# Optimization experiments

Hardware: AMD Instinct MI355X
Metric: run time of the kernel (lower is better)

Reference implementation:

```python
import jax, jax.numpy as jnp
import numpy as np

N_EMBD, D_INNER, DT_RANK, D_CONV, D_STATE, SEQ_LEN = 2048, 4096, 128, 4, 16, 2048


def setup_inputs() -> dict:
    key = jax.random.key(0)
    ks = jax.random.split(key, 8)
    sc = lambda fan_in: 1.0 / np.sqrt(fan_in)
    x = jax.random.normal(ks[0], (SEQ_LEN, N_EMBD), dtype=jnp.float32)
    in_proj_w = jax.random.normal(ks[1], (2 * D_INNER, N_EMBD), jnp.float32) * sc(N_EMBD)
    in_proj_b = jnp.zeros((2 * D_INNER,), jnp.float32)
    conv_w = jax.random.normal(ks[2], (D_INNER, 1, D_CONV), jnp.float32) * sc(D_CONV)
    conv_b = jnp.zeros((D_INNER,), jnp.float32)
    ssm_in_w = jax.random.normal(ks[3], (DT_RANK + 2 * D_STATE, D_INNER), jnp.float32) * sc(D_INNER)
    delta_w = jax.random.normal(ks[4], (D_INNER, DT_RANK), jnp.float32) * sc(DT_RANK)
    # A_log init exactly as module: repeat(arange(1,d_state+1), d_inner).reshape(d_inner,d_state)
    A_log = jnp.log(jnp.repeat(jnp.arange(1, D_STATE + 1), D_INNER).reshape(D_INNER, D_STATE).astype(jnp.float32))
    D = jnp.ones((D_INNER,), jnp.float32)
    out_w = jax.random.normal(ks[5], (N_EMBD, D_INNER), jnp.float32) * sc(D_INNER)
    out_b = jnp.zeros((N_EMBD,), jnp.float32)
    return {"x": x, "in_proj_w": in_proj_w, "in_proj_b": in_proj_b, "conv_w": conv_w,
            "conv_b": conv_b, "ssm_in_w": ssm_in_w, "delta_w": delta_w, "A_log": A_log,
            "D": D, "out_w": out_w, "out_b": out_b}


def selective_scan(u, delta, A, B, C, D):
    # u, delta: (L, di); A: (di, ds); B, C: (L, ds); D: (di,)
    dA = jnp.exp(delta[:, :, None] * A[None, :, :])                # (L, di, ds)
    dBu = delta[:, :, None] * B[:, None, :] * u[:, :, None]        # (L, di, ds)

    def step(h, inp):
        dA_t, dBu_t, C_t = inp
        h = dA_t * h + dBu_t                                       # (di, ds)
        y = jnp.einsum('ds,s->d', h, C_t)
        return h, y

    h0 = jnp.zeros((u.shape[1], A.shape[1]), u.dtype)
    _, ys = jax.lax.scan(step, h0, (dA, dBu, C))
    return ys + u * D                                              # (L, di)


def mamba_block(x, in_proj_w, in_proj_b, conv_w, conv_b, ssm_in_w, delta_w, A_log, D, out_w, out_b):
    L = x.shape[0]
    xr = x @ in_proj_w.T + in_proj_b                               # (L, 2*di)
    xi, res = jnp.split(xr, 2, axis=-1)
    # depthwise causal conv1d: left-pad d_conv-1 (== first L outputs of symmetric pad)
    xc = jax.lax.conv_general_dilated(
        xi.T[None],                                                # (1, di, L)
        conv_w,                                                    # (di, 1, k)
        window_strides=(1,), padding=[(D_CONV - 1, 0)],
        feature_group_count=D_INNER)[0] + conv_b[:, None]
    xc = jax.nn.silu(xc.T)                                         # (L, di)
    # SSM
    A = -jnp.exp(A_log)
    dbc = xc @ ssm_in_w.T                                          # (L, dt_rank + 2*ds)
    delta, B, C = jnp.split(dbc, [DT_RANK, DT_RANK + D_STATE], axis=-1)
    delta = jax.nn.softplus(delta @ delta_w.T)                     # (L, di)
    y = selective_scan(xc, delta, A, B, C, D)
    y = y * jax.nn.silu(res)
    return y @ out_w.T + out_b                                     # (L, n_embd)


def reference(x, in_proj_w, in_proj_b, conv_w, conv_b, ssm_in_w, delta_w, A_log, D, out_w, out_b):
    return mamba_block(x, in_proj_w, in_proj_b, conv_w, conv_b, ssm_in_w, delta_w, A_log, D, out_w, out_b)
```

## Files before the change

### kernel.cpp

```cpp
#include <hip/hip_runtime.h>
#include <cstdint>
#include <cstddef>


typedef __bf16 bf16x8 __attribute__((ext_vector_type(8)));
typedef float f32x4 __attribute__((ext_vector_type(4)));

#define GLDS16(g, l)                                        \
  __builtin_amdgcn_global_load_lds(                         \
      (__attribute__((address_space(1))) void*)(g),         \
      (__attribute__((address_space(3))) void*)(l), 16, 0, 0)

#define FENCE() asm volatile("" ::: "memory")
#define BARRIER()                      \
  do {                                 \
    FENCE();                           \
    __builtin_amdgcn_s_barrier();      \
    FENCE();                           \
  } while (0)

static __device__ __forceinline__ unsigned short f2b(float f) {
  unsigned int x = __builtin_bit_cast(unsigned int, f);
  x += 0x7fffu + ((x >> 16) & 1u);
  return (unsigned short)(x >> 16);
}

static __device__ __forceinline__ float b2f(unsigned short u) {
  return __builtin_bit_cast(float, (unsigned int)u << 16);
}

static __device__ __forceinline__ float sigmoidf_fast(float x) {
  return 1.0f / (1.0f + __expf(-x));
}

struct CastArgs {
  const float* src[5];
  unsigned short* dst[5];
  int n4[5];
};

__global__ __launch_bounds__(256) void cast_multi(CastArgs a) {
  const int stride = gridDim.x * 256;
  const int t = blockIdx.x * 256 + threadIdx.x;
#pragma unroll
  for (int k = 0; k < 5; ++k) {
    const float4* src = reinterpret_cast<const float4*>(a.src[k]);
    ushort4* dst = reinterpret_cast<ushort4*>(a.dst[k]);
    const int n4 = a.n4[k];
    for (int i = t; i < n4; i += stride) {
      float4 v = src[i];
      ushort4 o;
      o.x = f2b(v.x); o.y = f2b(v.y); o.z = f2b(v.z); o.w = f2b(v.w);
      dst[i] = o;
    }
  }
}

template <int MODE>
__global__ __launch_bounds__(512) void gemm256_bt(
    const unsigned short* __restrict__ A, const unsigned short* __restrict__ B,
    float* __restrict__ Cp, unsigned short* __restrict__ xib,
    unsigned short* __restrict__ rsb, const float* __restrict__ bias,
    int M, int N, int K, int Kslice) {
  __shared__ __align__(16) unsigned short lds[65536];
  const int tid = threadIdx.x;
  const int l = tid & 63;
  const int w = tid >> 6;
  const int wr = w >> 2;
  const int wc = w & 3;

  const int nwg = gridDim.x * gridDim.y;
  const int q = nwg >> 3;
  int flat = blockIdx.x + gridDim.x * blockIdx.y;
  flat = (flat & 7) * q + (flat >> 3);
  const int bx = flat % gridDim.x;
  const int by = flat / gridDim.x;

  const long brow = (long)bx * 256;
  const long bcol = (long)by * 256;
  const int ks = blockIdx.z;
  const int NT = Kslice >> 6;

  f32x4 acc[8][4] = {};

  const unsigned short* Ab = A + (size_t)brow * K + (size_t)ks * Kslice;
  const unsigned short* Bb = B + (size_t)bcol * K + (size_t)ks * Kslice;
  size_t soff[4];
  int doff[4];
#pragma unroll
  for (int i = 0; i < 4; ++i) {
    int idx = i * 512 + tid;
    int r = idx >> 3, s = idx & 7;
    soff[i] = (size_t)r * K + (size_t)((s ^ (r & 7)) << 3);
    doff[i] = idx * 8;
  }

  auto stage = [&](int kt, int buf) {
    const int k0 = kt << 6;
#pragma unroll
    for (int i = 0; i < 4; ++i)
      GLDS16(Ab + soff[i] + k0, &lds[buf * 32768 + doff[i]]);
#pragma unroll
    for (int i = 0; i < 4; ++i)
      GLDS16(Bb + soff[i] + k0, &lds[buf * 32768 + 16384 + doff[i]]);
  };

  const int hi = l >> 4, lo7 = l & 7;
  const int sw0 = ((0 + hi) ^ lo7) << 3;
  const int sw1 = ((4 + hi) ^ lo7) << 3;
  const int rowA = wr * 128 + (l & 15);
  const int colB = wc * 64 + (l & 15);

  stage(0, 0);
  stage(1, 1);

  int buf = 0;
  for (int kt = 0; kt < NT; ++kt) {
    const bool last = (kt == NT - 1);
    if (last) {
      asm volatile("s_waitcnt vmcnt(0)" ::: "memory");
    } else {
      asm volatile("s_waitcnt vmcnt(8)" ::: "memory");
    }
    BARRIER();
    const int bb = buf * 32768;
    bf16x8 a0[8], b0[4];
#pragma unroll
    for (int m = 0; m < 8; ++m)
      a0[m] = *reinterpret_cast<const bf16x8*>(&lds[bb + (rowA + m * 16) * 64 + sw0]);
#pragma unroll
    for (int n = 0; n < 4; ++n)
      b0[n] = *reinterpret_cast<const bf16x8*>(&lds[bb + 16384 + (colB + n * 16) * 64 + sw0]);
    __builtin_amdgcn_s_setprio(1);
#pragma unroll
    for (int m = 0; m < 8; ++m)
#pragma unroll
      for (int n = 0; n < 4; ++n)
        acc[m][n] = __builtin_amdgcn_mfma_f32_16x16x32_bf16(a0[m], b0[n], acc[m][n], 0, 0, 0);
    __builtin_amdgcn_s_setprio(0);
    bf16x8 a1[8], b1[4];
#pragma unroll
    for (int m = 0; m < 8; ++m)
      a1[m] = *reinterpret_cast<const bf16x8*>(&lds[bb + (rowA + m * 16) * 64 + sw1]);
#pragma unroll
    for (int n = 0; n < 4; ++n)
      b1[n] = *reinterpret_cast<const bf16x8*>(&lds[bb + 16384 + (colB + n * 16) * 64 + sw1]);
    asm volatile("s_waitcnt lgkmcnt(0)" ::: "memory");
    __builtin_amdgcn_sched_barrier(0);
    BARRIER();
    if (kt + 2 < NT) stage(kt + 2, buf);
    __builtin_amdgcn_s_setprio(1);
#pragma unroll
    for (int m = 0; m < 8; ++m)
#pragma unroll
      for (int n = 0; n < 4; ++n)
        acc[m][n] = __builtin_amdgcn_mfma_f32_16x16x32_bf16(a1[m], b1[n], acc[m][n], 0, 0, 0);
    __builtin_amdgcn_s_setprio(0);
    buf ^= 1;
  }

  const long r0 = brow + wr * 128 + (l >> 4) * 4;
  const long c0 = bcol + wc * 64 + (l & 15);
  if (MODE == 1) {
    float* Cb = Cp + (size_t)ks * M * N;
#pragma unroll
    for (int m = 0; m < 8; ++m)
#pragma unroll
      for (int n = 0; n < 4; ++n) {
        long col = c0 + n * 16;
#pragma unroll
        for (int r = 0; r < 4; ++r)
          Cb[(r0 + m * 16 + r) * (long)N + col] = acc[m][n][r];
      }
  } else {
#pragma unroll
    for (int m = 0; m < 8; ++m)
#pragma unroll
      for (int n = 0; n < 4; ++n) {
        long col = c0 + n * 16;
        float bv = bias[col];
        const bool isres = col >= 4096;
        long cc = isres ? col - 4096 : col;
#pragma unroll
        for (int r = 0; r < 4; ++r) {
          float v = acc[m][n][r] + bv;
          if (isres) {
            float s = v * sigmoidf_fast(v);
            rsb[(r0 + m * 16 + r) * 4096 + cc] = f2b(s);
          } else {
            xib[(r0 + m * 16 + r) * 4096 + cc] = f2b(v);
          }
        }
      }
  }
}

__global__ __launch_bounds__(256) void reduce4_bias(
    const float* __restrict__ part, const float* __restrict__ bias,
    float* __restrict__ out, int n4) {
  int stride = gridDim.x * 256;
  for (int f = blockIdx.x * 256 + threadIdx.x; f < n4; f += stride) {
    float4 s0 = reinterpret_cast<const float4*>(part)[f];
    float4 s1 = reinterpret_cast<const float4*>(part + 4194304ull)[f];
    float4 s2 = reinterpret_cast<const float4*>(part + 8388608ull)[f];
    float4 s3 = reinterpret_cast<const float4*>(part + 12582912ull)[f];
    float4 bv = reinterpret_cast<const float4*>(bias)[f & 511];
    float4 o;
    o.x = s0.x + s1.x + s2.x + s3.x + bv.x;
    o.y = s0.y + s1.y + s2.y + s3.y + bv.y;
    o.z = s0.z + s1.z + s2.z + s3.z + bv.z;
    o.w = s0.w + s1.w + s2.w + s3.w + bv.w;
    reinterpret_cast<float4*>(out)[f] = o;
  }
}

__global__ __launch_bounds__(256) void gemm_bt_sp(
    const unsigned short* __restrict__ A, const unsigned short* __restrict__ B,
    float* __restrict__ C, int M, int N, int K) {
  __shared__ __align__(16) unsigned short lA[128 * 32];
  __shared__ __align__(16) unsigned short lB[128 * 32];
  const int tid = threadIdx.x;
  const int l = tid & 63;
  const int w = tid >> 6;
  const int wr = w >> 1, wc = w & 1;
  const long brow = (long)blockIdx.x * 128;
  const long bcol = (long)blockIdx.y * 128;

  f32x4 acc[4][4] = {};

  const int srow = tid >> 2;
  const int scol = (tid & 3) * 8;

  const unsigned short* Ab = A + (size_t)brow * K;
  const unsigned short* Bb = B + (size_t)bcol * K;

  for (int k0 = 0; k0 < K; k0 += 32) {
#pragma unroll
    for (int j = 0; j < 2; ++j) {
      GLDS16(Ab + (size_t)(j * 64 + srow) * K + k0 + scol, &lA[j * 2048 + tid * 8]);
      GLDS16(Bb + (size_t)(j * 64 + srow) * K + k0 + scol, &lB[j * 2048 + tid * 8]);
    }
    __syncthreads();
    bf16x8 af[4], bfr[4];
#pragma unroll
    for (int mt = 0; mt < 4; ++mt)
      af[mt] = *reinterpret_cast<const bf16x8*>(
          &lA[(wr * 64 + mt * 16 + (l & 15)) * 32 + (l >> 4) * 8]);
#pragma unroll
    for (int nt = 0; nt < 4; ++nt)
      bfr[nt] = *reinterpret_cast<const bf16x8*>(
          &lB[(wc * 64 + nt * 16 + (l & 15)) * 32 + (l >> 4) * 8]);
#pragma unroll
    for (int mt = 0; mt < 4; ++mt)
#pragma unroll
      for (int nt = 0; nt < 4; ++nt)
        acc[mt][nt] = __builtin_amdgcn_mfma_f32_16x16x32_bf16(
            af[mt], bfr[nt], acc[mt][nt], 0, 0, 0);
    __syncthreads();
  }

  const long r0 = brow + wr * 64 + ((l >> 4) * 4);
  const long c0 = bcol + wc * 64 + (l & 15);
#pragma unroll
  for (int mt = 0; mt < 4; ++mt) {
#pragma unroll
    for (int nt = 0; nt < 4; ++nt) {
      long col = c0 + nt * 16;
#pragma unroll
      for (int r = 0; r < 4; ++r) {
        long row = r0 + mt * 16 + r;
        float v = acc[mt][nt][r];
        v = (v > 20.0f) ? v : log1pf(__expf(v));
        C[row * (long)N + col] = v;
      }
    }
  }
}

__global__ __launch_bounds__(256) void conv_silu_k(
    const unsigned short* __restrict__ xib, const float* __restrict__ cw,
    const float* __restrict__ cb, unsigned short* __restrict__ xcb) {
  const int d = blockIdx.x * 256 + threadIdx.x;
  const int t0 = blockIdx.y * 128;
  const float4 wv = *reinterpret_cast<const float4*>(cw + (size_t)d * 4);
  const float bv = cb[d];
  float xm3 = (t0 >= 3) ? b2f(xib[(size_t)(t0 - 3) * 4096 + d]) : 0.0f;
  float xm2 = (t0 >= 2) ? b2f(xib[(size_t)(t0 - 2) * 4096 + d]) : 0.0f;
  float xm1 = (t0 >= 1) ? b2f(xib[(size_t)(t0 - 1) * 4096 + d]) : 0.0f;
  for (int tt = 0; tt < 128; ++tt) {
    const size_t t = (size_t)t0 + tt;
    float xt = b2f(xib[t * 4096 + d]);
    float a = bv + wv.x * xm3 + wv.y * xm2 + wv.z * xm1 + wv.w * xt;
    float s = a * sigmoidf_fast(a);
    xcb[t * 4096 + d] = f2b(s);
    xm3 = xm2; xm2 = xm1; xm1 = xt;
  }
}

__global__ __launch_bounds__(256) void gemm_dbc(
    const unsigned short* __restrict__ A, const unsigned short* __restrict__ B,
    float* __restrict__ part) {
  __shared__ __align__(16) unsigned short lA[64 * 32];
  __shared__ __align__(16) unsigned short lB[160 * 32];
  const int tid = threadIdx.x;
  const int l = tid & 63, w = tid >> 6;
  const int brow = blockIdx.x * 64;
  const int ks = blockIdx.y;
  const int K = 4096;
  f32x4 acc[10] = {};
  const int srow = tid >> 2, scol = (tid & 3) * 8;
  for (int k0 = ks * 512; k0 < ks * 512 + 512; k0 += 32) {
    GLDS16(A + (size_t)(brow + srow) * K + k0 + scol, &lA[tid * 8]);
#pragma unroll
    for (int j = 0; j < 3; ++j) {
      int li = j * 256 + tid;
      if (li < 640) {
        GLDS16(B + (size_t)(li >> 2) * K + k0 + (li & 3) * 8, &lB[li * 8]);
      }
    }
    __syncthreads();
    bf16x8 af = *reinterpret_cast<const bf16x8*>(
        &lA[(w * 16 + (l & 15)) * 32 + (l >> 4) * 8]);
#pragma unroll
    for (int nt = 0; nt < 10; ++nt) {
      bf16x8 bfr = *reinterpret_cast<const bf16x8*>(
          &lB[(nt * 16 + (l & 15)) * 32 + (l >> 4) * 8]);
      acc[nt] = __builtin_amdgcn_mfma_f32_16x16x32_bf16(af, bfr, acc[nt], 0, 0, 0);
    }
    __syncthreads();
  }
  const int r0 = brow + w * 16 + (l >> 4) * 4;
  const int c = l & 15;
#pragma unroll
  for (int nt = 0; nt < 10; ++nt)
#pragma unroll
    for (int r = 0; r < 4; ++r)
      part[((size_t)ks * 2048 + r0 + r) * 160 + nt * 16 + c] = acc[nt][r];
}

__global__ __launch_bounds__(256) void reduce_dbc(
    const float* __restrict__ part, unsigned short* __restrict__ drb,
    float* __restrict__ bc) {
  int idx = blockIdx.x * 256 + threadIdx.x;
  float s = 0.0f;
#pragma unroll
  for (int k = 0; k < 8; ++k) s += part[(size_t)k * 2048 * 160 + idx];
  int row = idx / 160, col = idx - row * 160;
  if (col < 128) drb[row * 128 + col] = f2b(s);
  else bc[row * 32 + (col - 128)] = s;
}

__global__ __launch_bounds__(256) void scan_passA(
    const float* __restrict__ delta, const unsigned short* __restrict__ xcb,
    const float* __restrict__ bc, const float* __restrict__ alog,
    float* __restrict__ P, float* __restrict__ S) {
  __shared__ float lbc[1024];
  const int d = blockIdx.x * 256 + threadIdx.x;
  const int c = blockIdx.y;
  const int t0 = c * 32;
#pragma unroll
  for (int j = 0; j < 4; ++j) {
    int idx = j * 256 + threadIdx.x;
    lbc[idx] = bc[(size_t)t0 * 32 + idx];
  }
  __syncthreads();
  float a[16], h[16], p[16];
#pragma unroll
  for (int s = 0; s < 16; ++s) {
    a[s] = -__expf(alog[(size_t)d * 16 + s]);
    h[s] = 0.0f;
    p[s] = 1.0f;
  }
  for (int tt = 0; tt < 32; ++tt) {
    float dt = delta[(size_t)(t0 + tt) * 4096 + d];
    float u = b2f(xcb[(size_t)(t0 + tt) * 4096 + d]);
    float du = dt * u;
#pragma unroll
    for (int s = 0; s < 16; ++s) {
      float e = __expf(dt * a[s]);
      h[s] = e * h[s] + du * lbc[tt * 32 + s];
      p[s] *= e;
    }
  }
  size_t o = ((size_t)c * 4096 + d) * 16;
#pragma unroll
  for (int s = 0; s < 16; s += 4) {
    *reinterpret_cast<float4*>(&P[o + s]) = make_float4(p[s], p[s + 1], p[s + 2], p[s + 3]);
    *reinterpret_cast<float4*>(&S[o + s]) = make_float4(h[s], h[s + 1], h[s + 2], h[s + 3]);
  }
}

__global__ __launch_bounds__(256) void scan_passB(
    float* __restrict__ P, const float* __restrict__ S) {
  const int idx = blockIdx.x * 256 + threadIdx.x;
  float h = 0.0f;
  for (int c = 0; c < 64; ++c) {
    size_t o = (size_t)c * 65536 + idx;
    float p = P[o], sv = S[o];
    P[o] = h;
    h = p * h + sv;
  }
}

__global__ __launch_bounds__(256) void scan_passC(
    const float* __restrict__ delta, const unsigned short* __restrict__ xcb,
    const float* __restrict__ bc, const float* __restrict__ alog,
    const float* __restrict__ hst, const float* __restrict__ Dp,
    const unsigned short* __restrict__ rsb, unsigned short* __restrict__ yb) {
  __shared__ float lbc[1024];
  const int d = blockIdx.x * 256 + threadIdx.x;
  const int c = blockIdx.y;
  const int t0 = c * 32;
#pragma unroll
  for (int j = 0; j < 4; ++j) {
    int idx = j * 256 + threadIdx.x;
    lbc[idx] = bc[(size_t)t0 * 32 + idx];
  }
  __syncthreads();
  float a[16], h[16];
  size_t o = ((size_t)c * 4096 + d) * 16;
#pragma unroll
  for (int s = 0; s < 16; ++s) {
    a[s] = -__expf(alog[(size_t)d * 16 + s]);
    h[s] = hst[o + s];
  }
  const float Dv = Dp[d];
  for (int tt = 0; tt < 32; ++tt) {
    float dt = delta[(size_t)(t0 + tt) * 4096 + d];
    float u = b2f(xcb[(size_t)(t0 + tt) * 4096 + d]);
    float du = dt * u;
    float y = 0.0f;
#pragma unroll
    for (int s = 0; s < 16; ++s) {
      float e = __expf(dt * a[s]);
      h[s] = e * h[s] + du * lbc[tt * 32 + s];
      y += h[s] * lbc[tt * 32 + 16 + s];
    }
    float rs = b2f(rsb[(size_t)(t0 + tt) * 4096 + d]);
    float v = (y + u * Dv) * rs;
    yb[(size_t)(t0 + tt) * 4096 + d] = f2b(v);
  }
}

extern "C" void kernel_launch(void* const* d_in, const int* in_sizes, int n_in,
                              void* d_out, int out_size, void* d_ws, size_t ws_size,
                              hipStream_t stream) {
  const float* x    = (const float*)d_in[0];
  const float* w1   = (const float*)d_in[1];
  const float* b1   = (const float*)d_in[2];
  const float* cw   = (const float*)d_in[3];
  const float* cb   = (const float*)d_in[4];
  const float* w2   = (const float*)d_in[5];
  const float* w3   = (const float*)d_in[6];
  const float* alog = (const float*)d_in[7];
  const float* Dp   = (const float*)d_in[8];
  const float* w4   = (const float*)d_in[9];
  const float* b4   = (const float*)d_in[10];
  float* out = (float*)d_out;

  char* ws = (char*)d_ws;
  size_t off = 0;
  auto alloc = [&](size_t b) {
    size_t o = off;
    off += (b + 255) & ~(size_t)255;
    return o;
  };
  unsigned short* w1b = (unsigned short*)(ws + alloc(2ull * 8192 * 2048));
  unsigned short* xb  = (unsigned short*)(ws + alloc(2ull * 2048 * 2048));
  unsigned short* w2b = (unsigned short*)(ws + alloc(2ull * 160 * 4096));
  unsigned short* w3b = (unsigned short*)(ws + alloc(2ull * 4096 * 128));
  unsigned short* w4b = (unsigned short*)(ws + alloc(2ull * 2048 * 4096));
  unsigned short* xib = (unsigned short*)(ws + alloc(2ull * 2048 * 4096));
  unsigned short* rsb = (unsigned short*)(ws + alloc(2ull * 2048 * 4096));
  unsigned short* xcb = (unsigned short*)(ws + alloc(2ull * 2048 * 4096));
  unsigned short* drb = (unsigned short*)(ws + alloc(2ull * 2048 * 128));
  float* bcb  = (float*)(ws + alloc(4ull * 2048 * 32));
  float* delta = (float*)(ws + alloc(4ull * 2048 * 4096));
  float* P = (float*)(ws + alloc(4ull * 64 * 4096 * 16));
  float* S = (float*)(ws + alloc(4ull * 64 * 4096 * 16));
  float* part  = delta;
  unsigned short* yb = xib;
  float* part4 = delta;

  if (ws_size < off) return;

  CastArgs ca;
  ca.src[0] = w1; ca.dst[0] = w1b; ca.n4[0] = 8192 * 2048 / 4;
  ca.src[1] = x;  ca.dst[1] = xb;  ca.n4[1] = 2048 * 2048 / 4;
  ca.src[2] = w2; ca.dst[2] = w2b; ca.n4[2] = 160 * 4096 / 4;
  ca.src[3] = w3; ca.dst[3] = w3b; ca.n4[3] = 4096 * 128 / 4;
  ca.src[4] = w4; ca.dst[4] = w4b; ca.n4[4] = 2048 * 4096 / 4;
  cast_multi<<<2048, 256, 0, stream>>>(ca);

  gemm256_bt<2><<<dim3(8, 32, 1), 512, 0, stream>>>(
      xb, w1b, nullptr, xib, rsb, b1, 2048, 8192, 2048, 2048);
  conv_silu_k<<<dim3(16, 16), 256, 0, stream>>>(xib, cw, cb, xcb);
  gemm_dbc<<<dim3(32, 8), 256, 0, stream>>>(xcb, w2b, part);
  reduce_dbc<<<1280, 256, 0, stream>>>(part, drb, bcb);
  gemm_bt_sp<<<dim3(16, 32), 256, 0, stream>>>(drb, w3b, delta, 2048, 4096, 128);
  scan_passA<<<dim3(16, 64), 256, 0, stream>>>(delta, xcb, bcb, alog, P, S);
  scan_passB<<<256, 256, 0, stream>>>(P, S);
  scan_passC<<<dim3(16, 64), 256, 0, stream>>>(delta, xcb, bcb, alog, P, Dp, rsb, yb);
  gemm256_bt<1><<<dim3(8, 8, 4), 512, 0, stream>>>(
      yb, w4b, part4, nullptr, nullptr, nullptr, 2048, 2048, 4096, 1024);
  reduce4_bias<<<1024, 256, 0, stream>>>(part4, b4, out, 2048 * 2048 / 4);
}
```

Measured before the change: 315.2 us.

## Restructure bf16 GEMM mainloop into quadrant-phased half-tile loads and MFMAs

Replaces the two-phase K-split mainloop of the 256x256 GEMM with a four-phase schedule. Each phase loads a 128-row half of A or B into LDS and reads fragments for one output quadrant, so MFMA work on one quadrant overlaps the global-to-LDS loads of the next half-tiles. Warps now own interleaved 64x32 sub-blocks across all four quadrants instead of a contiguous 128x64 block, so the epilogue index math changes to match. This adds more barriers per K-step and more complex wait counts, which risks correctness and extra synchronisation stalls.

New measurement: 329.8 us. +4.6%, slower.

```diff
diff --git a/kernel.cpp b/kernel.cpp
--- a/kernel.cpp
+++ b/kernel.cpp
@@ -85,113 +85,149 @@
 
   const unsigned short* Ab = A + (size_t)brow * K + (size_t)ks * Kslice;
   const unsigned short* Bb = B + (size_t)bcol * K + (size_t)ks * Kslice;
-  size_t soff[4];
-  int doff[4];
-#pragma unroll
-  for (int i = 0; i < 4; ++i) {
+
+  size_t soff[2];
+  int doff[2];
+#pragma unroll
+  for (int i = 0; i < 2; ++i) {
     int idx = i * 512 + tid;
     int r = idx >> 3, s = idx & 7;
     soff[i] = (size_t)r * K + (size_t)((s ^ (r & 7)) << 3);
     doff[i] = idx * 8;
   }
 
-  auto stage = [&](int kt, int buf) {
-    const int k0 = kt << 6;
-#pragma unroll
-    for (int i = 0; i < 4; ++i)
-      GLDS16(Ab + soff[i] + k0, &lds[buf * 32768 + doff[i]]);
-#pragma unroll
-    for (int i = 0; i < 4; ++i)
-      GLDS16(Bb + soff[i] + k0, &lds[buf * 32768 + 16384 + doff[i]]);
+  auto stA = [&](int kt, int mh) {
+    const unsigned short* src = Ab + (size_t)(mh * 128) * K + (kt << 6);
+    const int reg = (kt & 1) * 32768 + mh * 8192;
+#pragma unroll
+    for (int i = 0; i < 2; ++i) GLDS16(src + soff[i], &lds[reg + doff[i]]);
   };
-
-  const int hi = l >> 4, lo7 = l & 7;
-  const int sw0 = ((0 + hi) ^ lo7) << 3;
-  const int sw1 = ((4 + hi) ^ lo7) << 3;
-  const int rowA = wr * 128 + (l & 15);
-  const int colB = wc * 64 + (l & 15);
-
-  stage(0, 0);
-  stage(1, 1);
-
-  int buf = 0;
+  auto stB = [&](int kt, int nh) {
+    const unsigned short* src = Bb + (size_t)(nh * 128) * K + (kt << 6);
+    const int reg = (kt & 1) * 32768 + 16384 + nh * 8192;
+#pragma unroll
+    for (int i = 0; i < 2; ++i) GLDS16(src + soff[i], &lds[reg + doff[i]]);
+  };
+
+  const int la = l & 15, hi = l >> 4;
+  int swz[2];
+  swz[0] = (hi ^ (la & 7)) * 8;
+  swz[1] = ((hi + 4) ^ (la & 7)) * 8;
+  int rowAoff[4], rowBoff[2];
+#pragma unroll
+  for (int qq = 0; qq < 4; ++qq) rowAoff[qq] = (wr * 64 + qq * 16 + la) * 64;
+#pragma unroll
+  for (int jj = 0; jj < 2; ++jj) rowBoff[jj] = (wc * 32 + jj * 16 + la) * 64;
+
+  bf16x8 afr[4][2], bfr[2][2];
+
+  auto readA = [&](int kt, int mh) {
+    const int base = (kt & 1) * 32768 + mh * 8192;
+#pragma unroll
+    for (int qq = 0; qq < 4; ++qq)
+#pragma unroll
+      for (int kk = 0; kk < 2; ++kk)
+        afr[qq][kk] = *reinterpret_cast<const bf16x8*>(&lds[base + rowAoff[qq] + swz[kk]]);
+  };
+  auto readB = [&](int kt, int nh) {
+    const int base = (kt & 1) * 32768 + 16384 + nh * 8192;
+#pragma unroll
+    for (int jj = 0; jj < 2; ++jj)
+#pragma unroll
+      for (int kk = 0; kk < 2; ++kk)
+        bfr[jj][kk] = *reinterpret_cast<const bf16x8*>(&lds[base + rowBoff[jj] + swz[kk]]);
+  };
+
+  auto mmaQ = [&](int mh, int nh) {
+    __builtin_amdgcn_s_setprio(1);
+#pragma unroll
+    for (int qq = 0; qq < 4; ++qq)
+#pragma unroll
+      for (int jj = 0; jj < 2; ++jj)
+#pragma unroll
+        for (int kk = 0; kk < 2; ++kk)
+          acc[mh * 4 + qq][nh * 2 + jj] = __builtin_amdgcn_mfma_f32_16x16x32_bf16(
+              afr[qq][kk], bfr[jj][kk], acc[mh * 4 + qq][nh * 2 + jj], 0, 0, 0);
+    __builtin_amdgcn_s_setprio(0);
+  };
+
+  stA(0, 0); stB(0, 0); stA(0, 1); stB(0, 1); stB(1, 0); stA(1, 1);
+  asm volatile("s_waitcnt vmcnt(8)" ::: "memory");
+  BARRIER();
+
   for (int kt = 0; kt < NT; ++kt) {
-    const bool last = (kt == NT - 1);
-    if (last) {
-      asm volatile("s_waitcnt vmcnt(0)" ::: "memory");
-    } else {
-      asm volatile("s_waitcnt vmcnt(8)" ::: "memory");
-    }
-    BARRIER();
-    const int bb = buf * 32768;
-    bf16x8 a0[8], b0[4];
-#pragma unroll
-    for (int m = 0; m < 8; ++m)
-      a0[m] = *reinterpret_cast<const bf16x8*>(&lds[bb + (rowA + m * 16) * 64 + sw0]);
-#pragma unroll
-    for (int n = 0; n < 4; ++n)
-      b0[n] = *reinterpret_cast<const bf16x8*>(&lds[bb + 16384 + (colB + n * 16) * 64 + sw0]);
-    __builtin_amdgcn_s_setprio(1);
-#pragma unroll
-    for (int m = 0; m < 8; ++m)
-#pragma unroll
-      for (int n = 0; n < 4; ++n)
-        acc[m][n] = __builtin_amdgcn_mfma_f32_16x16x32_bf16(a0[m], b0[n], acc[m][n], 0, 0, 0);
-    __builtin_amdgcn_s_setprio(0);
-    bf16x8 a1[8], b1[4];
-#pragma unroll
-    for (int m = 0; m < 8; ++m)
-      a1[m] = *reinterpret_cast<const bf16x8*>(&lds[bb + (rowA + m * 16) * 64 + sw1]);
-#pragma unroll
-    for (int n = 0; n < 4; ++n)
-      b1[n] = *reinterpret_cast<const bf16x8*>(&lds[bb + 16384 + (colB + n * 16) * 64 + sw1]);
+    const bool tail = (kt >= NT - 2);
+    if (kt + 1 < NT) stA(kt + 1, 0);
+    readA(kt, 0); readB(kt, 0);
+    BARRIER();
     asm volatile("s_waitcnt lgkmcnt(0)" ::: "memory");
     __builtin_amdgcn_sched_barrier(0);
-    BARRIER();
-    if (kt + 2 < NT) stage(kt + 2, buf);
-    __builtin_amdgcn_s_setprio(1);
-#pragma unroll
-    for (int m = 0; m < 8; ++m)
-#pragma unroll
-      for (int n = 0; n < 4; ++n)
-        acc[m][n] = __builtin_amdgcn_mfma_f32_16x16x32_bf16(a1[m], b1[n], acc[m][n], 0, 0, 0);
-    __builtin_amdgcn_s_setprio(0);
-    buf ^= 1;
-  }
-
-  const long r0 = brow + wr * 128 + (l >> 4) * 4;
-  const long c0 = bcol + wc * 64 + (l & 15);
+    mmaQ(0, 0);
+    BARRIER();
+    if (tail) asm volatile("s_waitcnt vmcnt(0)" ::: "memory");
+    else      asm volatile("s_waitcnt vmcnt(6)" ::: "memory");
+    if (kt + 1 < NT) stB(kt + 1, 1);
+    readA(kt, 1);
+    BARRIER();
+    asm volatile("s_waitcnt lgkmcnt(0)" ::: "memory");
+    __builtin_amdgcn_sched_barrier(0);
+    mmaQ(1, 0);
+    BARRIER();
+    if (kt + 2 < NT) stB(kt + 2, 0);
+    readB(kt, 1);
+    BARRIER();
+    asm volatile("s_waitcnt lgkmcnt(0)" ::: "memory");
+    __builtin_amdgcn_sched_barrier(0);
+    mmaQ(1, 1);
+    BARRIER();
+    if (tail) asm volatile("s_waitcnt vmcnt(0)" ::: "memory");
+    else      asm volatile("s_waitcnt vmcnt(4)" ::: "memory");
+    if (kt + 2 < NT) stA(kt + 2, 1);
+    readA(kt, 0);
+    BARRIER();
+    asm volatile("s_waitcnt lgkmcnt(0)" ::: "memory");
+    __builtin_amdgcn_sched_barrier(0);
+    mmaQ(0, 1);
+    BARRIER();
+  }
+
+  const long rbase = brow + wr * 64 + (l >> 4) * 4;
+  const long cbase = bcol + wc * 32 + (l & 15);
   if (MODE == 1) {
     float* Cb = Cp + (size_t)ks * M * N;
 #pragma unroll
-    for (int m = 0; m < 8; ++m)
+    for (int m = 0; m < 8; ++m) {
+      const long r0 = rbase + (m >> 2) * 128 + (m & 3) * 16;
 #pragma unroll
       for (int n = 0; n < 4; ++n) {
-        long col = c0 + n * 16;
+        const long col = cbase + (n >> 1) * 128 + (n & 1) * 16;
 #pragma unroll
         for (int r = 0; r < 4; ++r)
-          Cb[(r0 + m * 16 + r) * (long)N + col] = acc[m][n][r];
+          Cb[(r0 + r) * (long)N + col] = acc[m][n][r];
       }
+    }
   } else {
 #pragma unroll
-    for (int m = 0; m < 8; ++m)
+    for (int m = 0; m < 8; ++m) {
+      const long r0 = rbase + (m >> 2) * 128 + (m & 3) * 16;
 #pragma unroll
       for (int n = 0; n < 4; ++n) {
-        long col = c0 + n * 16;
-        float bv = bias[col];
+        const long col = cbase + (n >> 1) * 128 + (n & 1) * 16;
+        const float bv = bias[col];
         const bool isres = col >= 4096;
-        long cc = isres ? col - 4096 : col;
+        const long cc = isres ? col - 4096 : col;
 #pragma unroll
         for (int r = 0; r < 4; ++r) {
           float v = acc[m][n][r] + bv;
           if (isres) {
             float s = v * sigmoidf_fast(v);
-            rsb[(r0 + m * 16 + r) * 4096 + cc] = f2b(s);
+            rsb[(r0 + r) * 4096 + cc] = f2b(s);
           } else {
-            xib[(r0 + m * 16 + r) * 4096 + cc] = f2b(v);
+            xib[(r0 + r) * 4096 + cc] = f2b(v);
           }
         }
       }
+    }
   }
 }
 
```

## Replace split-K out-projection GEMM and reduction with 128x128 tile GEMM

Applied to the files above, without the earlier changes.

The final output projection used to run as a 4-way split-K 256-tile GEMM writing fp32 partials, followed by a separate reduction kernel that added the bias. It now uses a new 128x128-tile GEMM kernel with 512 threads and full K, which adds the bias in its epilogue and writes directly to the output. The kernel double-buffers global-to-LDS loads with swizzling and remaps block order in an XCD-aware way. This removes the partial-sum write/read traffic and one launch, at the cost of fewer blocks (256) each running a longer K loop.

Measured after the change: 304.3 us. -3.5%, faster.

```diff
diff --git a/kernel.cpp b/kernel.cpp
--- a/kernel.cpp
+++ b/kernel.cpp
@@ -195,22 +195,118 @@
   }
 }
 
-__global__ __launch_bounds__(256) void reduce4_bias(
-    const float* __restrict__ part, const float* __restrict__ bias,
-    float* __restrict__ out, int n4) {
-  int stride = gridDim.x * 256;
-  for (int f = blockIdx.x * 256 + threadIdx.x; f < n4; f += stride) {
-    float4 s0 = reinterpret_cast<const float4*>(part)[f];
-    float4 s1 = reinterpret_cast<const float4*>(part + 4194304ull)[f];
-    float4 s2 = reinterpret_cast<const float4*>(part + 8388608ull)[f];
-    float4 s3 = reinterpret_cast<const float4*>(part + 12582912ull)[f];
-    float4 bv = reinterpret_cast<const float4*>(bias)[f & 511];
-    float4 o;
-    o.x = s0.x + s1.x + s2.x + s3.x + bv.x;
-    o.y = s0.y + s1.y + s2.y + s3.y + bv.y;
-    o.z = s0.z + s1.z + s2.z + s3.z + bv.z;
-    o.w = s0.w + s1.w + s2.w + s3.w + bv.w;
-    reinterpret_cast<float4*>(out)[f] = o;
+__global__ __launch_bounds__(512) void gemm128_bt(
+    const unsigned short* __restrict__ A, const unsigned short* __restrict__ B,
+    float* __restrict__ C, const float* __restrict__ bias,
+    int M, int N, int K) {
+  __shared__ __align__(16) unsigned short lds[32768];
+  const int tid = threadIdx.x;
+  const int l = tid & 63;
+  const int w = tid >> 6;
+  const int wr = w >> 2;
+  const int wc = w & 3;
+
+  const int nwg = gridDim.x * gridDim.y;
+  const int q = nwg >> 3;
+  int flat = blockIdx.x + gridDim.x * blockIdx.y;
+  flat = (flat & 7) * q + (flat >> 3);
+  const int bx = flat % gridDim.x;
+  const int by = flat / gridDim.x;
+
+  const long brow = (long)bx * 128;
+  const long bcol = (long)by * 128;
+  const int NT = K >> 6;
+
+  f32x4 acc[4][2] = {};
+
+  const unsigned short* Ab = A + (size_t)brow * K;
+  const unsigned short* Bb = B + (size_t)bcol * K;
+  size_t soff[2];
+  int doff[2];
+#pragma unroll
+  for (int i = 0; i < 2; ++i) {
+    int idx = i * 512 + tid;
+    int r = idx >> 3, s = idx & 7;
+    soff[i] = (size_t)r * K + (size_t)((s ^ (r & 7)) << 3);
+    doff[i] = idx * 8;
+  }
+
+  auto stage = [&](int kt, int buf) {
+    const int k0 = kt << 6;
+#pragma unroll
+    for (int i = 0; i < 2; ++i)
+      GLDS16(Ab + soff[i] + k0, &lds[buf * 16384 + doff[i]]);
+#pragma unroll
+    for (int i = 0; i < 2; ++i)
+      GLDS16(Bb + soff[i] + k0, &lds[buf * 16384 + 8192 + doff[i]]);
+  };
+
+  const int hi = l >> 4, lo7 = l & 7;
+  const int sw0 = ((0 + hi) ^ lo7) << 3;
+  const int sw1 = ((4 + hi) ^ lo7) << 3;
+  const int rowA = wr * 64 + (l & 15);
+  const int colB = wc * 32 + (l & 15);
+
+  stage(0, 0);
+  stage(1, 1);
+
+  int buf = 0;
+  for (int kt = 0; kt < NT; ++kt) {
+    const bool last = (kt == NT - 1);
+    if (last) {
+      asm volatile("s_waitcnt vmcnt(0)" ::: "memory");
+    } else {
+      asm volatile("s_waitcnt vmcnt(4)" ::: "memory");
+    }
+    BARRIER();
+    const int bb = buf * 16384;
+    bf16x8 a0[4], b0[2];
+#pragma unroll
+    for (int m = 0; m < 4; ++m)
+      a0[m] = *reinterpret_cast<const bf16x8*>(&lds[bb + (rowA + m * 16) * 64 + sw0]);
+#pragma unroll
+    for (int n = 0; n < 2; ++n)
+      b0[n] = *reinterpret_cast<const bf16x8*>(&lds[bb + 8192 + (colB + n * 16) * 64 + sw0]);
+    __builtin_amdgcn_s_setprio(1);
+#pragma unroll
+    for (int m = 0; m < 4; ++m)
+#pragma unroll
+      for (int n = 0; n < 2; ++n)
+        acc[m][n] = __builtin_amdgcn_mfma_f32_16x16x32_bf16(a0[m], b0[n], acc[m][n], 0, 0, 0);
+    __builtin_amdgcn_s_setprio(0);
+    bf16x8 a1[4], b1[2];
+#pragma unroll
+    for (int m = 0; m < 4; ++m)
+      a1[m] = *reinterpret_cast<const bf16x8*>(&lds[bb + (rowA + m * 16) * 64 + sw1]);
+#pragma unroll
+    for (int n = 0; n < 2; ++n)
+      b1[n] = *reinterpret_cast<const bf16x8*>(&lds[bb + 8192 + (colB + n * 16) * 64 + sw1]);
+    asm volatile("s_waitcnt lgkmcnt(0)" ::: "memory");
+    __builtin_amdgcn_sched_barrier(0);
+    BARRIER();
+    if (kt + 2 < NT) stage(kt + 2, buf);
+    __builtin_amdgcn_s_setprio(1);
+#pragma unroll
+    for (int m = 0; m < 4; ++m)
+#pragma unroll
+      for (int n = 0; n < 2; ++n)
+        acc[m][n] = __builtin_amdgcn_mfma_f32_16x16x32_bf16(a1[m], b1[n], acc[m][n], 0, 0, 0);
+    __builtin_amdgcn_s_setprio(0);
+    buf ^= 1;
+  }
+
+  const long r0 = brow + wr * 64 + (l >> 4) * 4;
+  const long c0 = bcol + wc * 32 + (l & 15);
+#pragma unroll
+  for (int m = 0; m < 4; ++m) {
+#pragma unroll
+    for (int n = 0; n < 2; ++n) {
+      long col = c0 + n * 16;
+      float bv = bias[col];
+#pragma unroll
+      for (int r = 0; r < 4; ++r)
+        C[(r0 + m * 16 + r) * (long)N + col] = acc[m][n][r] + bv;
+    }
   }
 }
 
@@ -480,7 +576,6 @@
   float* S = (float*)(ws + alloc(4ull * 64 * 4096 * 16));
   float* part  = delta;
   unsigned short* yb = xib;
-  float* part4 = delta;
 
   if (ws_size < off) return;
 
@@ -501,7 +596,5 @@
   scan_passA<<<dim3(16, 64), 256, 0, stream>>>(delta, xcb, bcb, alog, P, S);
   scan_passB<<<256, 256, 0, stream>>>(P, S);
   scan_passC<<<dim3(16, 64), 256, 0, stream>>>(delta, xcb, bcb, alog, P, Dp, rsb, yb);
-  gemm256_bt<1><<<dim3(8, 8, 4), 512, 0, stream>>>(
-      yb, w4b, part4, nullptr, nullptr, nullptr, 2048, 2048, 4096, 1024);
-  reduce4_bias<<<1024, 256, 0, stream>>>(part4, b4, out, 2048 * 2048 / 4);
-}
+  gemm128_bt<<<dim3(16, 16), 512, 0, stream>>>(yb, w4b, out, b4, 2048, 2048, 4096);
+}
```
